# Optimization experiments

Measured on AMD Instinct MI355X. Metric: run time of the kernel, lower is better.

The kernel has to match this reference:

```python
import jax, jax.numpy as jnp
import numpy as np

EMBED_DIM = 2048
N_HEAD = 16
N_KV_HEAD = 4
HEAD_DIM = EMBED_DIM // N_HEAD  # 128
GROUP = N_HEAD // N_KV_HEAD     # 4
SCALE = HEAD_DIM ** -0.5
B, T = 2, 2048


def setup_inputs() -> dict:
    key = jax.random.key(0)
    ks = jax.random.split(key, 5)
    s = 0.02
    # weights stored as [in, out] (y = x @ W); equivalent to torch Linear W.T
    return {
        "x": jax.random.normal(ks[0], (B, T, EMBED_DIM), jnp.float32),
        "Wq": jax.random.normal(ks[1], (EMBED_DIM, EMBED_DIM), jnp.float32) * s,
        "Wk": jax.random.normal(ks[2], (EMBED_DIM, N_KV_HEAD * HEAD_DIM), jnp.float32) * s,
        "Wv": jax.random.normal(ks[3], (EMBED_DIM, N_KV_HEAD * HEAD_DIM), jnp.float32) * s,
        "Wo": jax.random.normal(ks[4], (EMBED_DIM, EMBED_DIM), jnp.float32) * s,
    }


def reference(x, Wq, Wk, Wv, Wo):
    # Prefill path (T>1, no cache): GQA causal attention, eval mode (dropout=0).
    Bq, Tq, C = x.shape
    q = (x @ Wq).reshape(Bq, Tq, N_HEAD, HEAD_DIM).transpose(0, 2, 1, 3)      # (B,Hq,T,D)
    k = (x @ Wk).reshape(Bq, Tq, N_KV_HEAD, HEAD_DIM).transpose(0, 2, 1, 3)  # (B,Hkv,T,D)
    v = (x @ Wv).reshape(Bq, Tq, N_KV_HEAD, HEAD_DIM).transpose(0, 2, 1, 3)
    # expand_kv: each kv head repeated GROUP times consecutively
    k = jnp.repeat(k, GROUP, axis=1)  # (B,Hq,T,D)
    v = jnp.repeat(v, GROUP, axis=1)
    scores = jnp.einsum("bhqd,bhkd->bhqk", q, k) * SCALE
    causal = jnp.tril(jnp.ones((Tq, Tq), dtype=bool))
    scores = jnp.where(causal[None, None], scores, jnp.finfo(scores.dtype).min)
    probs = jax.nn.softmax(scores, axis=-1)
    atten = jnp.einsum("bhqk,bhkd->bhqd", probs, v)
    atten = atten.transpose(0, 2, 1, 3).reshape(Bq, Tq, C)
    out = atten @ Wo
    return out
```

## Files before the change

kernel.cpp:

```cpp
#include <hip/hip_runtime.h>

typedef unsigned short u16;
typedef unsigned int   u32;
typedef __attribute__((ext_vector_type(4))) float  f32x4;
typedef __attribute__((ext_vector_type(8))) __bf16 bf16x8;

#define EMBED 2048
#define NH    16
#define NKV   4
#define HD    128
#define TT    2048
#define BB    2
#define MROWS (BB*TT)
#define QSCALE 0.08838834764831845f

#define QELEMS ((size_t)BB*NH*TT*HD)
#define KELEMS ((size_t)BB*NKV*TT*HD)

static __device__ __forceinline__ u16 f2b(float f){
  union { float f; u32 u; } v; v.f = f;
  u32 u = v.u;
  u32 r = u + 0x7FFFu + ((u >> 16) & 1u);
  return (u16)(r >> 16);
}

__global__ __launch_bounds__(256) void cvt_f32_bf16(const float* __restrict__ in,
                                                    u16* __restrict__ out, int n4){
  int i = blockIdx.x * 256 + threadIdx.x;
  if (i >= n4) return;
  float4 v = ((const float4*)in)[i];
  uint2 o;
  o.x = (u32)f2b(v.x) | ((u32)f2b(v.y) << 16);
  o.y = (u32)f2b(v.z) | ((u32)f2b(v.w) << 16);
  ((uint2*)out)[i] = o;
}

__global__ __launch_bounds__(256) void trans_w2(const float* __restrict__ in0, u16* __restrict__ out0,
                                                const float* __restrict__ in1, u16* __restrict__ out1,
                                                int R, int C){
  const float* in = blockIdx.z ? in1 : in0;
  u16*        out = blockIdx.z ? out1 : out0;
  __shared__ u16 tile[32][33];
  int c0 = blockIdx.x * 32, r0 = blockIdx.y * 32;
  int tx = threadIdx.x & 31, ty = threadIdx.x >> 5;
  #pragma unroll
  for (int j = 0; j < 32; j += 8)
    tile[ty + j][tx] = f2b(in[(size_t)(r0 + ty + j) * C + c0 + tx]);
  __syncthreads();
  #pragma unroll
  for (int j = 0; j < 32; j += 8)
    out[(size_t)(c0 + ty + j) * R + r0 + tx] = tile[tx][ty + j];
}

__global__ __launch_bounds__(256) void trans_v(const u16* __restrict__ in,
                                               u16* __restrict__ out){
  __shared__ u16 tile[32][33];
  int d0 = (blockIdx.x & 3) * 32;
  int t0 = ((blockIdx.x >> 2) & 63) * 32;
  int bh = blockIdx.x >> 8;
  const u16* ip = in  + (size_t)bh * TT * HD;
  u16*       op = out + (size_t)bh * TT * HD;
  int tx = threadIdx.x & 31, ty = threadIdx.x >> 5;
  #pragma unroll
  for (int j = 0; j < 32; j += 8)
    tile[ty + j][tx] = ip[(size_t)(t0 + ty + j) * HD + d0 + tx];
  __syncthreads();
  #pragma unroll
  for (int j = 0; j < 32; j += 8)
    op[(size_t)(d0 + ty + j) * TT + t0 + tx] = tile[tx][ty + j];
}

template<int EPI>
__global__ __launch_bounds__(256)
void gemm_bt(const u16* __restrict__ A, const u16* __restrict__ Bt,
             void* __restrict__ outp, int N, int K){
  __shared__ __align__(16) u16 As[2][128*32];
  __shared__ __align__(16) u16 Bs[2][128*32];
  int tid  = threadIdx.x;
  int lane = tid & 63, w = tid >> 6;
  int nwg = gridDim.x;
  int bid = blockIdx.x;
  bid = (bid & 7) * (nwg >> 3) + (bid >> 3);
  int nbn  = N >> 7;
  int brow = (bid / nbn) * 128;
  int bcol = (bid % nbn) * 128;

  auto stage = [&](int buf, int kt){
    #pragma unroll
    for (int j = 0; j < 2; ++j){
      int boff  = w * 2048 + j * 1024;
      int chunk = (boff >> 4) + lane;
      int row   = chunk >> 2;
      int cko   = chunk & 3;
      const u16* ga = A  + (size_t)(brow + row) * K + kt + cko * 8;
      const u16* gb = Bt + (size_t)(bcol + row) * K + kt + cko * 8;
      __builtin_amdgcn_global_load_lds((__attribute__((address_space(1))) void*)(void*)ga,
          (__attribute__((address_space(3))) void*)(void*)(&As[buf][boff >> 1]), 16, 0, 0);
      __builtin_amdgcn_global_load_lds((__attribute__((address_space(1))) void*)(void*)gb,
          (__attribute__((address_space(3))) void*)(void*)(&Bs[buf][boff >> 1]), 16, 0, 0);
    }
  };

  int lr = lane & 15, lg = lane >> 4, lk = lg * 8;
  int wr = (w >> 1) * 64, wc = (w & 1) * 64;

  f32x4 acc[4][4];
  #pragma unroll
  for (int m = 0; m < 4; ++m)
    #pragma unroll
    for (int n = 0; n < 4; ++n)
      #pragma unroll
      for (int r = 0; r < 4; ++r) acc[m][n][r] = 0.f;

  int NT = K >> 5;
  stage(0, 0);
  asm volatile("s_waitcnt vmcnt(0)" ::: "memory");
  __syncthreads();
  int cur = 0;
  for (int t = 0; t < NT; ++t){
    if (t + 1 < NT) stage(cur ^ 1, (t + 1) * 32);
    const u16* as = As[cur];
    const u16* bs = Bs[cur];
    bf16x8 af[4], bfv[4];
    #pragma unroll
    for (int m = 0; m < 4; ++m) af[m]  = *(const bf16x8*)(as + (wr + m*16 + lr)*32 + lk);
    #pragma unroll
    for (int n = 0; n < 4; ++n) bfv[n] = *(const bf16x8*)(bs + (wc + n*16 + lr)*32 + lk);
    #pragma unroll
    for (int m = 0; m < 4; ++m)
      #pragma unroll
      for (int n = 0; n < 4; ++n)
        acc[m][n] = __builtin_amdgcn_mfma_f32_16x16x32_bf16(af[m], bfv[n], acc[m][n], 0, 0, 0);
    asm volatile("s_waitcnt vmcnt(0)" ::: "memory");
    __syncthreads();
    cur ^= 1;
  }

  if (EPI == 0){
    float* o = (float*)outp;
    #pragma unroll
    for (int m = 0; m < 4; ++m)
      #pragma unroll
      for (int r = 0; r < 4; ++r){
        int rowg = brow + wr + m*16 + lg*4 + r;
        float* orow = o + (size_t)rowg * N + bcol + wc + lr;
        #pragma unroll
        for (int n = 0; n < 4; ++n) orow[n*16] = acc[m][n][r];
      }
  } else {
    u16* qb = (u16*)outp;
    u16* kb = qb + QELEMS;
    u16* vb = kb + KELEMS;
    int hb = bcol >> 7;
    int b  = brow >> 11;
    u16* hp; float s;
    if (hb < 16)      { hp = qb + ((size_t)(b*NH  +  hb     )) * TT * HD; s = QSCALE; }
    else if (hb < 20) { hp = kb + ((size_t)(b*NKV + (hb-16))) * TT * HD; s = 1.0f; }
    else              { hp = vb + ((size_t)(b*NKV + (hb-20))) * TT * HD; s = 1.0f; }
    #pragma unroll
    for (int m = 0; m < 4; ++m)
      #pragma unroll
      for (int r = 0; r < 4; ++r){
        int t = (brow + wr + m*16 + lg*4 + r) & (TT - 1);
        #pragma unroll
        for (int n = 0; n < 4; ++n){
          int d = wc + n*16 + lr;
          hp[(size_t)t * HD + d] = f2b(acc[m][n][r] * s);
        }
      }
  }
}

__global__ __launch_bounds__(256)
void attn_kernel(const u16* __restrict__ qb, const u16* __restrict__ kb,
                 const u16* __restrict__ vtb, u16* __restrict__ ob){
  __shared__ __align__(16) u16 Ks[2][64*128];
  __shared__ __align__(16) u16 Vs[2][128*64];
  __shared__ __align__(16) u16 pl[4][16*88];
  int tid = threadIdx.x, lane = tid & 63, w = tid >> 6;
  int nwg = gridDim.x;
  int bid = blockIdx.x;
  bid = (bid & 7) * (nwg >> 3) + (bid >> 3);
  int pair = bid & 15;
  int h    = (bid >> 4) & 15;
  int b    = bid >> 8;
  int hkv  = h >> 2;
  int lr = lane & 15, lg = lane >> 4, lk = lg * 8;
  int sw = (lr & 7) << 3;

  const u16* qbase = qb  + ((size_t)b * NH  + h  ) * TT * HD;
  const u16* kbase = kb  + ((size_t)b * NKV + hkv) * TT * HD;
  const u16* vbase = vtb + ((size_t)b * NKV + hkv) * HD * TT;

  auto stage = [&](int buf, int kt){
    #pragma unroll
    for (int i = 0; i < 4; ++i){
      int c  = i * 256 + tid;
      int ub = (i * 256 + w * 64) * 8;
      int kr = c >> 4, kc = (c & 15) ^ (kr & 7);
      const u16* gk = kbase + (size_t)(kt * 64 + kr) * HD + kc * 8;
      __builtin_amdgcn_global_load_lds((__attribute__((address_space(1))) void*)(void*)gk,
          (__attribute__((address_space(3))) void*)(void*)(&Ks[buf][ub]), 16, 0, 0);
      int vr = c >> 3, vc = (c & 7) ^ (vr & 7);
      const u16* gv = vbase + (size_t)vr * TT + kt * 64 + vc * 8;
      __builtin_amdgcn_global_load_lds((__attribute__((address_space(1))) void*)(void*)gv,
          (__attribute__((address_space(3))) void*)(void*)(&Vs[buf][ub]), 16, 0, 0);
    }
  };

  __bf16* plw = (__bf16*)pl[w];

  for (int half = 0; half < 2; ++half){
    int qt = half ? (31 - pair) : pair;
    int q0 = qt * 64 + w * 16;

    bf16x8 aq[4];
    #pragma unroll
    for (int s = 0; s < 4; ++s)
      aq[s] = *(const bf16x8*)(qbase + (size_t)(q0 + lr) * HD + s*32 + lk);

    f32x4 o_acc[8];
    #pragma unroll
    for (int dt = 0; dt < 8; ++dt)
      #pragma unroll
      for (int r = 0; r < 4; ++r) o_acc[dt][r] = 0.f;
    float mrow[4], lrow[4];
    #pragma unroll
    for (int r = 0; r < 4; ++r){ mrow[r] = -1e30f; lrow[r] = 0.f; }

    __builtin_amdgcn_s_barrier();
    stage(0, 0);
    int cur = 0;
    for (int kt = 0; kt <= qt; ++kt){
      __builtin_amdgcn_s_barrier();
      if (kt < qt){
        stage(cur ^ 1, kt + 1);
        asm volatile("s_waitcnt vmcnt(8)" ::: "memory");
      } else {
        asm volatile("s_waitcnt vmcnt(0)" ::: "memory");
      }
      __builtin_amdgcn_s_barrier();

      const u16* ks = Ks[cur];
      f32x4 sc[4];
      #pragma unroll
      for (int c = 0; c < 4; ++c)
        #pragma unroll
        for (int r = 0; r < 4; ++r) sc[c][r] = 0.f;
      __builtin_amdgcn_s_setprio(1);
      #pragma unroll
      for (int c = 0; c < 4; ++c){
        const u16* kp = ks + (c*16 + lr) * 128;
        #pragma unroll
        for (int s = 0; s < 4; ++s){
          bf16x8 kf = *(const bf16x8*)(kp + (((s*32) + lk) ^ sw));
          sc[c] = __builtin_amdgcn_mfma_f32_16x16x32_bf16(aq[s], kf, sc[c], 0, 0, 0);
        }
      }
      __builtin_amdgcn_s_setprio(0);
      if (kt == qt){
        #pragma unroll
        for (int c = 0; c < 4; ++c){
          int kvg = kt*64 + c*16 + lr;
          #pragma unroll
          for (int r = 0; r < 4; ++r){
            int qg = q0 + lg*4 + r;
            if (kvg > qg) sc[c][r] = -1e30f;
          }
        }
      }
      float tmv[4];
      #pragma unroll
      for (int r = 0; r < 4; ++r){
        float tm = fmaxf(fmaxf(sc[0][r], sc[1][r]), fmaxf(sc[2][r], sc[3][r]));
        tm = fmaxf(tm, __shfl_xor(tm, 1));
        tm = fmaxf(tm, __shfl_xor(tm, 2));
        tm = fmaxf(tm, __shfl_xor(tm, 4));
        tm = fmaxf(tm, __shfl_xor(tm, 8));
        tmv[r] = tm;
      }
      bool need = (tmv[0] > mrow[0] + 8.f) || (tmv[1] > mrow[1] + 8.f) ||
                  (tmv[2] > mrow[2] + 8.f) || (tmv[3] > mrow[3] + 8.f);
      if (__any(need ? 1 : 0)){
        #pragma unroll
        for (int r = 0; r < 4; ++r){
          float mnew  = fmaxf(mrow[r], tmv[r]);
          float alpha = __expf(mrow[r] - mnew);
          mrow[r] = mnew;
          lrow[r] *= alpha;
          #pragma unroll
          for (int dt = 0; dt < 8; ++dt) o_acc[dt][r] *= alpha;
        }
      }
      #pragma unroll
      for (int r = 0; r < 4; ++r){
        float rs = 0.f;
        #pragma unroll
        for (int c = 0; c < 4; ++c){
          float p = __expf(sc[c][r] - mrow[r]);
          rs += p;
          plw[(lg*4 + r)*88 + c*16 + lr] = (__bf16)p;
        }
        rs += __shfl_xor(rs, 1); rs += __shfl_xor(rs, 2);
        rs += __shfl_xor(rs, 4); rs += __shfl_xor(rs, 8);
        lrow[r] += rs;
      }
      asm volatile("s_waitcnt lgkmcnt(0)" ::: "memory");
      bf16x8 pa[2];
      #pragma unroll
      for (int kk = 0; kk < 2; ++kk)
        pa[kk] = *(const bf16x8*)((const u16*)plw + lr*88 + kk*32 + lk);
      const u16* vs = Vs[cur];
      __builtin_amdgcn_s_setprio(1);
      #pragma unroll
      for (int dt = 0; dt < 8; ++dt){
        const u16* vp = vs + (dt*16 + lr) * 64;
        #pragma unroll
        for (int kk = 0; kk < 2; ++kk){
          bf16x8 vf = *(const bf16x8*)(vp + (((kk*32) + lk) ^ sw));
          o_acc[dt] = __builtin_amdgcn_mfma_f32_16x16x32_bf16(pa[kk], vf, o_acc[dt], 0, 0, 0);
        }
      }
      __builtin_amdgcn_s_setprio(0);
      cur ^= 1;
    }
    #pragma unroll
    for (int r = 0; r < 4; ++r){
      float inv = 1.0f / lrow[r];
      int t = q0 + lg*4 + r;
      size_t base = ((size_t)b * TT + t) * EMBED + h * HD;
      #pragma unroll
      for (int dt = 0; dt < 8; ++dt)
        ob[base + dt*16 + lr] = f2b(o_acc[dt][r] * inv);
    }
  }
}

extern "C" void kernel_launch(void* const* d_in, const int* in_sizes, int n_in,
                              void* d_out, int out_size, void* d_ws, size_t ws_size,
                              hipStream_t stream){
  const float* x  = (const float*)d_in[0];
  const float* Wq = (const float*)d_in[1];
  const float* Wk = (const float*)d_in[2];
  const float* Wv = (const float*)d_in[3];
  const float* Wo = (const float*)d_in[4];

  char* ws = (char*)d_ws;
  size_t off = 0;
  auto alloc = [&](size_t bytes){ void* p = ws + off; off += (bytes + 255) & ~(size_t)255; return p; };
  u16* xb    = (u16*)alloc((size_t)MROWS * EMBED * 2);
  u16* Wqkvt = (u16*)alloc((size_t)3072 * EMBED * 2);
  u16* Wot   = (u16*)alloc((size_t)EMBED * EMBED * 2);
  u16* qkv   = (u16*)alloc((QELEMS + 2*KELEMS) * 2);
  u16* vtb   = (u16*)alloc(KELEMS * 2);
  u16* ob    = (u16*)alloc((size_t)MROWS * EMBED * 2);

  u16* qb = qkv;
  u16* kb = qb + QELEMS;
  u16* vb = kb + KELEMS;

  cvt_f32_bf16<<<(MROWS*EMBED/4 + 255)/256, 256, 0, stream>>>(x, xb, MROWS*EMBED/4);
  trans_w2<<<dim3(EMBED/32, EMBED/32, 2), 256, 0, stream>>>(Wq, Wqkvt, Wo, Wot, EMBED, EMBED);
  trans_w2<<<dim3(512/32,   EMBED/32, 2), 256, 0, stream>>>(Wk, Wqkvt + (size_t)2048*EMBED,
                                                            Wv, Wqkvt + (size_t)2560*EMBED, EMBED, 512);

  gemm_bt<2><<<(MROWS/128)*(3072/128), 256, 0, stream>>>(xb, Wqkvt, qkv, 3072, EMBED);
  trans_v<<<4*64*BB*NKV, 256, 0, stream>>>(vb, vtb);

  attn_kernel<<<BB*NH*16, 256, 0, stream>>>(qb, kb, vtb, ob);

  gemm_bt<0><<<(MROWS/128)*(EMBED/128), 256, 0, stream>>>(ob, Wot, d_out, EMBED, EMBED);
}
```

Baseline: 313.1 us.

## Use 256x256-tile 8-wave GEMM with swizzled LDS and phased prefetch for QKV

The QKV projection moves from the 128x128 tile, 4-wave GEMM to a new 256x256 tile kernel with 512 threads. It uses a two-half K=64 step, XOR-swizzled LDS layout, prefetch split across barriered phases, and s_setprio around the MFMA blocks. The larger tile doubles reuse per LDS load and cuts global traffic, and interleaving the loads with MFMA is meant to hide latency. In exchange it uses more LDS and registers, launches only 192 workgroups, which leaves the 256 CUs under-filled, and adds more barriers. The output GEMM keeps the old kernel, now de-templated.

```diff
diff --git a/kernel.cpp b/kernel.cpp
--- a/kernel.cpp
+++ b/kernel.cpp
@@ -16,6 +16,9 @@
 
 #define QELEMS ((size_t)BB*NH*TT*HD)
 #define KELEMS ((size_t)BB*NKV*TT*HD)
+
+#define AS1(p) (__attribute__((address_space(1))) void*)(void*)(p)
+#define AS3(p) (__attribute__((address_space(3))) void*)(void*)(p)
 
 static __device__ __forceinline__ u16 f2b(float f){
   union { float f; u32 u; } v; v.f = f;
@@ -70,7 +73,6 @@
     op[(size_t)(d0 + ty + j) * TT + t0 + tx] = tile[tx][ty + j];
 }
 
-template<int EPI>
 __global__ __launch_bounds__(256)
 void gemm_bt(const u16* __restrict__ A, const u16* __restrict__ Bt,
              void* __restrict__ outp, int N, int K){
@@ -94,10 +96,8 @@
       int cko   = chunk & 3;
       const u16* ga = A  + (size_t)(brow + row) * K + kt + cko * 8;
       const u16* gb = Bt + (size_t)(bcol + row) * K + kt + cko * 8;
-      __builtin_amdgcn_global_load_lds((__attribute__((address_space(1))) void*)(void*)ga,
-          (__attribute__((address_space(3))) void*)(void*)(&As[buf][boff >> 1]), 16, 0, 0);
-      __builtin_amdgcn_global_load_lds((__attribute__((address_space(1))) void*)(void*)gb,
-          (__attribute__((address_space(3))) void*)(void*)(&Bs[buf][boff >> 1]), 16, 0, 0);
+      __builtin_amdgcn_global_load_lds(AS1(ga), AS3(&As[buf][boff >> 1]), 16, 0, 0);
+      __builtin_amdgcn_global_load_lds(AS1(gb), AS3(&Bs[buf][boff >> 1]), 16, 0, 0);
     }
   };
 
@@ -136,39 +136,152 @@
     cur ^= 1;
   }
 
-  if (EPI == 0){
-    float* o = (float*)outp;
+  float* o = (float*)outp;
+  #pragma unroll
+  for (int m = 0; m < 4; ++m)
+    #pragma unroll
+    for (int r = 0; r < 4; ++r){
+      int rowg = brow + wr + m*16 + lg*4 + r;
+      float* orow = o + (size_t)rowg * N + bcol + wc + lr;
+      #pragma unroll
+      for (int n = 0; n < 4; ++n) orow[n*16] = acc[m][n][r];
+    }
+}
+
+__global__ __launch_bounds__(512, 2)
+void gemm256_qkv(const u16* __restrict__ A, const u16* __restrict__ Bt,
+                 u16* __restrict__ qkv, int N, int K){
+  __shared__ __align__(16) u16 As[2][2][256*32];
+  __shared__ __align__(16) u16 Bs[2][2][256*32];
+  int tid = threadIdx.x, lane = tid & 63, w = tid >> 6;
+  int nwg = gridDim.x, bid = blockIdx.x;
+  bid = (bid & 7) * (nwg >> 3) + (bid >> 3);
+  int nbn  = N >> 8;
+  int brow = (bid / nbn) * 256;
+  int bcol = (bid % nbn) * 256;
+  int wm = w >> 2, wn = w & 3;
+  int lr = lane & 15, lg = lane >> 4;
+  int swz = (lg ^ ((lr >> 1) & 3)) << 3;
+
+  auto stage = [&](const u16* __restrict__ src, u16* dst, int rowbase, int kt, int kk){
+    #pragma unroll
+    for (int j = 0; j < 2; ++j){
+      int c = j * 512 + tid;
+      int row = c >> 2, cc = c & 3;
+      const u16* g = src + (size_t)(rowbase + row) * K + kt * 64 + kk * 32
+                         + ((cc ^ ((row >> 1) & 3)) * 8);
+      __builtin_amdgcn_global_load_lds(AS1(g), AS3(dst + (j * 512 + w * 64) * 8), 16, 0, 0);
+    }
+  };
+
+  f32x4 acc[8][4];
+  #pragma unroll
+  for (int m = 0; m < 8; ++m)
+    #pragma unroll
+    for (int n = 0; n < 4; ++n)
+      #pragma unroll
+      for (int r = 0; r < 4; ++r) acc[m][n][r] = 0.f;
+
+  int NT = K >> 6;
+  int arow = wm * 128 + lr;
+  int brw  = wn * 64 + lr;
+
+  stage(A,  As[0][0], brow, 0, 0);
+  stage(Bt, Bs[0][0], bcol, 0, 0);
+  stage(A,  As[0][1], brow, 0, 1);
+  stage(Bt, Bs[0][1], bcol, 0, 1);
+  asm volatile("s_waitcnt vmcnt(4)" ::: "memory");
+  __builtin_amdgcn_s_barrier();
+  asm volatile("" ::: "memory");
+
+  for (int t = 0; t < NT; ++t){
+    int buf = t & 1, nb = buf ^ 1;
+    bool pre = (t + 1 < NT);
+    const u16* a0 = As[buf][0]; const u16* b0 = Bs[buf][0];
+    const u16* a1 = As[buf][1]; const u16* b1 = Bs[buf][1];
+    bf16x8 bfr[4], af[4];
+
+    #pragma unroll
+    for (int n = 0; n < 4; ++n) bfr[n] = *(const bf16x8*)(b0 + (brw + n*16)*32 + swz);
+    #pragma unroll
+    for (int m = 0; m < 4; ++m) af[m]  = *(const bf16x8*)(a0 + (arow + m*16)*32 + swz);
+    if (pre) stage(A, As[nb][0], brow, t + 1, 0);
+    __builtin_amdgcn_s_barrier(); asm volatile("" ::: "memory");
+    __builtin_amdgcn_s_setprio(1);
     #pragma unroll
     for (int m = 0; m < 4; ++m)
       #pragma unroll
-      for (int r = 0; r < 4; ++r){
-        int rowg = brow + wr + m*16 + lg*4 + r;
-        float* orow = o + (size_t)rowg * N + bcol + wc + lr;
-        #pragma unroll
-        for (int n = 0; n < 4; ++n) orow[n*16] = acc[m][n][r];
-      }
-  } else {
-    u16* qb = (u16*)outp;
-    u16* kb = qb + QELEMS;
-    u16* vb = kb + KELEMS;
-    int hb = bcol >> 7;
-    int b  = brow >> 11;
-    u16* hp; float s;
-    if (hb < 16)      { hp = qb + ((size_t)(b*NH  +  hb     )) * TT * HD; s = QSCALE; }
-    else if (hb < 20) { hp = kb + ((size_t)(b*NKV + (hb-16))) * TT * HD; s = 1.0f; }
-    else              { hp = vb + ((size_t)(b*NKV + (hb-20))) * TT * HD; s = 1.0f; }
+      for (int n = 0; n < 4; ++n)
+        acc[m][n] = __builtin_amdgcn_mfma_f32_16x16x32_bf16(af[m], bfr[n], acc[m][n], 0, 0, 0);
+    __builtin_amdgcn_s_setprio(0);
+    __builtin_amdgcn_s_barrier(); asm volatile("" ::: "memory");
+
+    #pragma unroll
+    for (int m = 0; m < 4; ++m) af[m] = *(const bf16x8*)(a0 + (arow + (m+4)*16)*32 + swz);
+    if (pre) stage(Bt, Bs[nb][0], bcol, t + 1, 0);
+    __builtin_amdgcn_s_barrier(); asm volatile("" ::: "memory");
+    __builtin_amdgcn_s_setprio(1);
     #pragma unroll
     for (int m = 0; m < 4; ++m)
       #pragma unroll
-      for (int r = 0; r < 4; ++r){
-        int t = (brow + wr + m*16 + lg*4 + r) & (TT - 1);
-        #pragma unroll
-        for (int n = 0; n < 4; ++n){
-          int d = wc + n*16 + lr;
-          hp[(size_t)t * HD + d] = f2b(acc[m][n][r] * s);
-        }
-      }
+      for (int n = 0; n < 4; ++n)
+        acc[m+4][n] = __builtin_amdgcn_mfma_f32_16x16x32_bf16(af[m], bfr[n], acc[m+4][n], 0, 0, 0);
+    __builtin_amdgcn_s_setprio(0);
+    if (pre) asm volatile("s_waitcnt vmcnt(4)" ::: "memory");
+    else     asm volatile("s_waitcnt vmcnt(0)" ::: "memory");
+    __builtin_amdgcn_s_barrier(); asm volatile("" ::: "memory");
+
+    #pragma unroll
+    for (int n = 0; n < 4; ++n) bfr[n] = *(const bf16x8*)(b1 + (brw + n*16)*32 + swz);
+    #pragma unroll
+    for (int m = 0; m < 4; ++m) af[m]  = *(const bf16x8*)(a1 + (arow + m*16)*32 + swz);
+    if (pre) stage(A, As[nb][1], brow, t + 1, 1);
+    __builtin_amdgcn_s_barrier(); asm volatile("" ::: "memory");
+    __builtin_amdgcn_s_setprio(1);
+    #pragma unroll
+    for (int m = 0; m < 4; ++m)
+      #pragma unroll
+      for (int n = 0; n < 4; ++n)
+        acc[m][n] = __builtin_amdgcn_mfma_f32_16x16x32_bf16(af[m], bfr[n], acc[m][n], 0, 0, 0);
+    __builtin_amdgcn_s_setprio(0);
+    __builtin_amdgcn_s_barrier(); asm volatile("" ::: "memory");
+
+    #pragma unroll
+    for (int m = 0; m < 4; ++m) af[m] = *(const bf16x8*)(a1 + (arow + (m+4)*16)*32 + swz);
+    if (pre) stage(Bt, Bs[nb][1], bcol, t + 1, 1);
+    __builtin_amdgcn_s_barrier(); asm volatile("" ::: "memory");
+    __builtin_amdgcn_s_setprio(1);
+    #pragma unroll
+    for (int m = 0; m < 4; ++m)
+      #pragma unroll
+      for (int n = 0; n < 4; ++n)
+        acc[m+4][n] = __builtin_amdgcn_mfma_f32_16x16x32_bf16(af[m], bfr[n], acc[m+4][n], 0, 0, 0);
+    __builtin_amdgcn_s_setprio(0);
+    if (pre) asm volatile("s_waitcnt vmcnt(4)" ::: "memory");
+    __builtin_amdgcn_s_barrier(); asm volatile("" ::: "memory");
   }
+
+  u16* qb = qkv;
+  u16* kb = qb + QELEMS;
+  u16* vb = kb + KELEMS;
+  int colbase = bcol + wn * 64;
+  int hb = colbase >> 7;
+  int dbase = colbase & 127;
+  int b = brow >> 11;
+  u16* hp; float s;
+  if (hb < 16)      { hp = qb + ((size_t)(b*NH  +  hb     )) * TT * HD; s = QSCALE; }
+  else if (hb < 20) { hp = kb + ((size_t)(b*NKV + (hb-16))) * TT * HD; s = 1.0f; }
+  else              { hp = vb + ((size_t)(b*NKV + (hb-20))) * TT * HD; s = 1.0f; }
+  #pragma unroll
+  for (int m = 0; m < 8; ++m)
+    #pragma unroll
+    for (int r = 0; r < 4; ++r){
+      int trow = (brow + wm*128 + m*16 + lg*4 + r) & (TT - 1);
+      u16* orow = hp + (size_t)trow * HD + dbase + lr;
+      #pragma unroll
+      for (int n = 0; n < 4; ++n)
+        orow[n*16] = f2b(acc[m][n][r] * s);
+    }
 }
 
 __global__ __launch_bounds__(256)
@@ -199,12 +312,10 @@
       int ub = (i * 256 + w * 64) * 8;
       int kr = c >> 4, kc = (c & 15) ^ (kr & 7);
       const u16* gk = kbase + (size_t)(kt * 64 + kr) * HD + kc * 8;
-      __builtin_amdgcn_global_load_lds((__attribute__((address_space(1))) void*)(void*)gk,
-          (__attribute__((address_space(3))) void*)(void*)(&Ks[buf][ub]), 16, 0, 0);
+      __builtin_amdgcn_global_load_lds(AS1(gk), AS3(&Ks[buf][ub]), 16, 0, 0);
       int vr = c >> 3, vc = (c & 7) ^ (vr & 7);
       const u16* gv = vbase + (size_t)vr * TT + kt * 64 + vc * 8;
-      __builtin_amdgcn_global_load_lds((__attribute__((address_space(1))) void*)(void*)gv,
-          (__attribute__((address_space(3))) void*)(void*)(&Vs[buf][ub]), 16, 0, 0);
+      __builtin_amdgcn_global_load_lds(AS1(gv), AS3(&Vs[buf][ub]), 16, 0, 0);
     }
   };
 
@@ -364,10 +475,10 @@
   trans_w2<<<dim3(512/32,   EMBED/32, 2), 256, 0, stream>>>(Wk, Wqkvt + (size_t)2048*EMBED,
                                                             Wv, Wqkvt + (size_t)2560*EMBED, EMBED, 512);
 
-  gemm_bt<2><<<(MROWS/128)*(3072/128), 256, 0, stream>>>(xb, Wqkvt, qkv, 3072, EMBED);
+  gemm256_qkv<<<(MROWS/256)*(3072/256), 512, 0, stream>>>(xb, Wqkvt, qkv, 3072, EMBED);
   trans_v<<<4*64*BB*NKV, 256, 0, stream>>>(vb, vtb);
 
   attn_kernel<<<BB*NH*16, 256, 0, stream>>>(qb, kb, vtb, ob);
 
-  gemm_bt<0><<<(MROWS/128)*(EMBED/128), 256, 0, stream>>>(ob, Wot, d_out, EMBED, EMBED);
-}
+  gemm_bt<<<(MROWS/128)*(EMBED/128), 256, 0, stream>>>(ob, Wot, d_out, EMBED, EMBED);
+}
```

New measurement: 322.7 us. +3.1%, slower.

## Single-buffer attention LDS and launch one workgroup per query tile

Applied to the files above, without the earlier changes.

The attention kernel drops the double-buffered K/V shared-memory tiles in favour of a single buffer, roughly halving its LDS footprint so more workgroups can be resident per CU. It also stops pairing causal query tiles per workgroup and launches one workgroup per 64-row query tile, doubling the grid. The cost is that K/V loads for the next tile no longer overlap compute: each iteration stages, waits for all loads and barriers. Causal load imbalance across workgroups is now left to the hardware scheduler rather than the paired-tile scheme.

```diff
diff --git a/kernel.cpp b/kernel.cpp
--- a/kernel.cpp
+++ b/kernel.cpp
@@ -16,6 +16,10 @@
 
 #define QELEMS ((size_t)BB*NH*TT*HD)
 #define KELEMS ((size_t)BB*NKV*TT*HD)
+
+#define AS1(p) (__attribute__((address_space(1))) void*)(void*)(p)
+#define AS3(p) (__attribute__((address_space(3))) void*)(void*)(p)
+
 
 static __device__ __forceinline__ u16 f2b(float f){
   union { float f; u32 u; } v; v.f = f;
@@ -94,10 +98,8 @@
       int cko   = chunk & 3;
       const u16* ga = A  + (size_t)(brow + row) * K + kt + cko * 8;
       const u16* gb = Bt + (size_t)(bcol + row) * K + kt + cko * 8;
-      __builtin_amdgcn_global_load_lds((__attribute__((address_space(1))) void*)(void*)ga,
-          (__attribute__((address_space(3))) void*)(void*)(&As[buf][boff >> 1]), 16, 0, 0);
-      __builtin_amdgcn_global_load_lds((__attribute__((address_space(1))) void*)(void*)gb,
-          (__attribute__((address_space(3))) void*)(void*)(&Bs[buf][boff >> 1]), 16, 0, 0);
+      __builtin_amdgcn_global_load_lds(AS1(ga), AS3(&As[buf][boff >> 1]), 16, 0, 0);
+      __builtin_amdgcn_global_load_lds(AS1(gb), AS3(&Bs[buf][boff >> 1]), 16, 0, 0);
     }
   };
 
@@ -174,17 +176,17 @@
 __global__ __launch_bounds__(256)
 void attn_kernel(const u16* __restrict__ qb, const u16* __restrict__ kb,
                  const u16* __restrict__ vtb, u16* __restrict__ ob){
-  __shared__ __align__(16) u16 Ks[2][64*128];
-  __shared__ __align__(16) u16 Vs[2][128*64];
+  __shared__ __align__(16) u16 Ks[64*128];
+  __shared__ __align__(16) u16 Vs[128*64];
   __shared__ __align__(16) u16 pl[4][16*88];
   int tid = threadIdx.x, lane = tid & 63, w = tid >> 6;
   int nwg = gridDim.x;
   int bid = blockIdx.x;
   bid = (bid & 7) * (nwg >> 3) + (bid >> 3);
-  int pair = bid & 15;
-  int h    = (bid >> 4) & 15;
-  int b    = bid >> 8;
-  int hkv  = h >> 2;
+  int qt = bid & 31;
+  int h  = (bid >> 5) & 15;
+  int b  = bid >> 9;
+  int hkv = h >> 2;
   int lr = lane & 15, lg = lane >> 4, lk = lg * 8;
   int sw = (lr & 7) << 3;
 
@@ -192,147 +194,136 @@
   const u16* kbase = kb  + ((size_t)b * NKV + hkv) * TT * HD;
   const u16* vbase = vtb + ((size_t)b * NKV + hkv) * HD * TT;
 
-  auto stage = [&](int buf, int kt){
+  auto stage = [&](int kt){
     #pragma unroll
     for (int i = 0; i < 4; ++i){
       int c  = i * 256 + tid;
       int ub = (i * 256 + w * 64) * 8;
       int kr = c >> 4, kc = (c & 15) ^ (kr & 7);
       const u16* gk = kbase + (size_t)(kt * 64 + kr) * HD + kc * 8;
-      __builtin_amdgcn_global_load_lds((__attribute__((address_space(1))) void*)(void*)gk,
-          (__attribute__((address_space(3))) void*)(void*)(&Ks[buf][ub]), 16, 0, 0);
+      __builtin_amdgcn_global_load_lds(AS1(gk), AS3(&Ks[ub]), 16, 0, 0);
       int vr = c >> 3, vc = (c & 7) ^ (vr & 7);
       const u16* gv = vbase + (size_t)vr * TT + kt * 64 + vc * 8;
-      __builtin_amdgcn_global_load_lds((__attribute__((address_space(1))) void*)(void*)gv,
-          (__attribute__((address_space(3))) void*)(void*)(&Vs[buf][ub]), 16, 0, 0);
+      __builtin_amdgcn_global_load_lds(AS1(gv), AS3(&Vs[ub]), 16, 0, 0);
     }
   };
 
   __bf16* plw = (__bf16*)pl[w];
-
-  for (int half = 0; half < 2; ++half){
-    int qt = half ? (31 - pair) : pair;
-    int q0 = qt * 64 + w * 16;
-
-    bf16x8 aq[4];
-    #pragma unroll
-    for (int s = 0; s < 4; ++s)
-      aq[s] = *(const bf16x8*)(qbase + (size_t)(q0 + lr) * HD + s*32 + lk);
-
-    f32x4 o_acc[8];
-    #pragma unroll
-    for (int dt = 0; dt < 8; ++dt)
-      #pragma unroll
-      for (int r = 0; r < 4; ++r) o_acc[dt][r] = 0.f;
-    float mrow[4], lrow[4];
-    #pragma unroll
-    for (int r = 0; r < 4; ++r){ mrow[r] = -1e30f; lrow[r] = 0.f; }
-
-    __builtin_amdgcn_s_barrier();
-    stage(0, 0);
-    int cur = 0;
-    for (int kt = 0; kt <= qt; ++kt){
-      __builtin_amdgcn_s_barrier();
-      if (kt < qt){
-        stage(cur ^ 1, kt + 1);
-        asm volatile("s_waitcnt vmcnt(8)" ::: "memory");
-      } else {
-        asm volatile("s_waitcnt vmcnt(0)" ::: "memory");
-      }
-      __builtin_amdgcn_s_barrier();
-
-      const u16* ks = Ks[cur];
-      f32x4 sc[4];
-      #pragma unroll
-      for (int c = 0; c < 4; ++c)
-        #pragma unroll
-        for (int r = 0; r < 4; ++r) sc[c][r] = 0.f;
-      __builtin_amdgcn_s_setprio(1);
+  int q0 = qt * 64 + w * 16;
+
+  bf16x8 aq[4];
+  #pragma unroll
+  for (int s = 0; s < 4; ++s)
+    aq[s] = *(const bf16x8*)(qbase + (size_t)(q0 + lr) * HD + s*32 + lk);
+
+  f32x4 o_acc[8];
+  #pragma unroll
+  for (int dt = 0; dt < 8; ++dt)
+    #pragma unroll
+    for (int r = 0; r < 4; ++r) o_acc[dt][r] = 0.f;
+  float mrow[4], lrow[4];
+  #pragma unroll
+  for (int r = 0; r < 4; ++r){ mrow[r] = -1e30f; lrow[r] = 0.f; }
+
+  stage(0);
+  asm volatile("s_waitcnt vmcnt(0)" ::: "memory");
+  __builtin_amdgcn_s_barrier();
+
+  for (int kt = 0; kt <= qt; ++kt){
+    f32x4 sc[4];
+    #pragma unroll
+    for (int c = 0; c < 4; ++c)
+      #pragma unroll
+      for (int r = 0; r < 4; ++r) sc[c][r] = 0.f;
+    __builtin_amdgcn_s_setprio(1);
+    #pragma unroll
+    for (int c = 0; c < 4; ++c){
+      const u16* kp = Ks + (c*16 + lr) * 128;
+      #pragma unroll
+      for (int s = 0; s < 4; ++s){
+        bf16x8 kf = *(const bf16x8*)(kp + (((s*32) + lk) ^ sw));
+        sc[c] = __builtin_amdgcn_mfma_f32_16x16x32_bf16(aq[s], kf, sc[c], 0, 0, 0);
+      }
+    }
+    __builtin_amdgcn_s_setprio(0);
+    if (kt == qt){
       #pragma unroll
       for (int c = 0; c < 4; ++c){
-        const u16* kp = ks + (c*16 + lr) * 128;
-        #pragma unroll
-        for (int s = 0; s < 4; ++s){
-          bf16x8 kf = *(const bf16x8*)(kp + (((s*32) + lk) ^ sw));
-          sc[c] = __builtin_amdgcn_mfma_f32_16x16x32_bf16(aq[s], kf, sc[c], 0, 0, 0);
-        }
-      }
-      __builtin_amdgcn_s_setprio(0);
-      if (kt == qt){
-        #pragma unroll
-        for (int c = 0; c < 4; ++c){
-          int kvg = kt*64 + c*16 + lr;
-          #pragma unroll
-          for (int r = 0; r < 4; ++r){
-            int qg = q0 + lg*4 + r;
-            if (kvg > qg) sc[c][r] = -1e30f;
-          }
-        }
-      }
-      float tmv[4];
-      #pragma unroll
-      for (int r = 0; r < 4; ++r){
-        float tm = fmaxf(fmaxf(sc[0][r], sc[1][r]), fmaxf(sc[2][r], sc[3][r]));
-        tm = fmaxf(tm, __shfl_xor(tm, 1));
-        tm = fmaxf(tm, __shfl_xor(tm, 2));
-        tm = fmaxf(tm, __shfl_xor(tm, 4));
-        tm = fmaxf(tm, __shfl_xor(tm, 8));
-        tmv[r] = tm;
-      }
-      bool need = (tmv[0] > mrow[0] + 8.f) || (tmv[1] > mrow[1] + 8.f) ||
-                  (tmv[2] > mrow[2] + 8.f) || (tmv[3] > mrow[3] + 8.f);
-      if (__any(need ? 1 : 0)){
+        int kvg = kt*64 + c*16 + lr;
         #pragma unroll
         for (int r = 0; r < 4; ++r){
-          float mnew  = fmaxf(mrow[r], tmv[r]);
-          float alpha = __expf(mrow[r] - mnew);
-          mrow[r] = mnew;
-          lrow[r] *= alpha;
-          #pragma unroll
-          for (int dt = 0; dt < 8; ++dt) o_acc[dt][r] *= alpha;
+          int qg = q0 + lg*4 + r;
+          if (kvg > qg) sc[c][r] = -1e30f;
         }
       }
+    }
+    float tmv[4];
+    #pragma unroll
+    for (int r = 0; r < 4; ++r){
+      float tm = fmaxf(fmaxf(sc[0][r], sc[1][r]), fmaxf(sc[2][r], sc[3][r]));
+      tm = fmaxf(tm, __shfl_xor(tm, 1));
+      tm = fmaxf(tm, __shfl_xor(tm, 2));
+      tm = fmaxf(tm, __shfl_xor(tm, 4));
+      tm = fmaxf(tm, __shfl_xor(tm, 8));
+      tmv[r] = tm;
+    }
+    bool need = (tmv[0] > mrow[0] + 8.f) || (tmv[1] > mrow[1] + 8.f) ||
+                (tmv[2] > mrow[2] + 8.f) || (tmv[3] > mrow[3] + 8.f);
+    if (__any(need ? 1 : 0)){
       #pragma unroll
       for (int r = 0; r < 4; ++r){
-        float rs = 0.f;
+        float mnew  = fmaxf(mrow[r], tmv[r]);
+        float alpha = __expf(mrow[r] - mnew);
+        mrow[r] = mnew;
+        lrow[r] *= alpha;
         #pragma unroll
-        for (int c = 0; c < 4; ++c){
-          float p = __expf(sc[c][r] - mrow[r]);
-          rs += p;
-          plw[(lg*4 + r)*88 + c*16 + lr] = (__bf16)p;
-        }
-        rs += __shfl_xor(rs, 1); rs += __shfl_xor(rs, 2);
-        rs += __shfl_xor(rs, 4); rs += __shfl_xor(rs, 8);
-        lrow[r] += rs;
-      }
-      asm volatile("s_waitcnt lgkmcnt(0)" ::: "memory");
-      bf16x8 pa[2];
-      #pragma unroll
-      for (int kk = 0; kk < 2; ++kk)
-        pa[kk] = *(const bf16x8*)((const u16*)plw + lr*88 + kk*32 + lk);
-      const u16* vs = Vs[cur];
-      __builtin_amdgcn_s_setprio(1);
-      #pragma unroll
-      for (int dt = 0; dt < 8; ++dt){
-        const u16* vp = vs + (dt*16 + lr) * 64;
-        #pragma unroll
-        for (int kk = 0; kk < 2; ++kk){
-          bf16x8 vf = *(const bf16x8*)(vp + (((kk*32) + lk) ^ sw));
-          o_acc[dt] = __builtin_amdgcn_mfma_f32_16x16x32_bf16(pa[kk], vf, o_acc[dt], 0, 0, 0);
-        }
-      }
-      __builtin_amdgcn_s_setprio(0);
-      cur ^= 1;
+        for (int dt = 0; dt < 8; ++dt) o_acc[dt][r] *= alpha;
+      }
     }
     #pragma unroll
     for (int r = 0; r < 4; ++r){
-      float inv = 1.0f / lrow[r];
-      int t = q0 + lg*4 + r;
-      size_t base = ((size_t)b * TT + t) * EMBED + h * HD;
-      #pragma unroll
-      for (int dt = 0; dt < 8; ++dt)
-        ob[base + dt*16 + lr] = f2b(o_acc[dt][r] * inv);
-    }
+      float rs = 0.f;
+      #pragma unroll
+      for (int c = 0; c < 4; ++c){
+        float p = __expf(sc[c][r] - mrow[r]);
+        rs += p;
+        plw[(lg*4 + r)*88 + c*16 + lr] = (__bf16)p;
+      }
+      rs += __shfl_xor(rs, 1); rs += __shfl_xor(rs, 2);
+      rs += __shfl_xor(rs, 4); rs += __shfl_xor(rs, 8);
+      lrow[r] += rs;
+    }
+    asm volatile("s_waitcnt lgkmcnt(0)" ::: "memory");
+    bf16x8 pa[2];
+    #pragma unroll
+    for (int kk = 0; kk < 2; ++kk)
+      pa[kk] = *(const bf16x8*)((const u16*)plw + lr*88 + kk*32 + lk);
+    __builtin_amdgcn_s_setprio(1);
+    #pragma unroll
+    for (int dt = 0; dt < 8; ++dt){
+      const u16* vp = Vs + (dt*16 + lr) * 64;
+      #pragma unroll
+      for (int kk = 0; kk < 2; ++kk){
+        bf16x8 vf = *(const bf16x8*)(vp + (((kk*32) + lk) ^ sw));
+        o_acc[dt] = __builtin_amdgcn_mfma_f32_16x16x32_bf16(pa[kk], vf, o_acc[dt], 0, 0, 0);
+      }
+    }
+    __builtin_amdgcn_s_setprio(0);
+    if (kt < qt){
+      __builtin_amdgcn_s_barrier();
+      stage(kt + 1);
+      asm volatile("s_waitcnt vmcnt(0)" ::: "memory");
+      __builtin_amdgcn_s_barrier();
+    }
+  }
+  #pragma unroll
+  for (int r = 0; r < 4; ++r){
+    float inv = 1.0f / lrow[r];
+    int t = q0 + lg*4 + r;
+    size_t base = ((size_t)b * TT + t) * EMBED + h * HD;
+    #pragma unroll
+    for (int dt = 0; dt < 8; ++dt)
+      ob[base + dt*16 + lr] = f2b(o_acc[dt][r] * inv);
   }
 }
 
@@ -367,7 +358,7 @@
   gemm_bt<2><<<(MROWS/128)*(3072/128), 256, 0, stream>>>(xb, Wqkvt, qkv, 3072, EMBED);
   trans_v<<<4*64*BB*NKV, 256, 0, stream>>>(vb, vtb);
 
-  attn_kernel<<<BB*NH*16, 256, 0, stream>>>(qb, kb, vtb, ob);
+  attn_kernel<<<BB*NH*32, 256, 0, stream>>>(qb, kb, vtb, ob);
 
   gemm_bt<0><<<(MROWS/128)*(EMBED/128), 256, 0, stream>>>(ob, Wot, d_out, EMBED, EMBED);
 }
```

After: 341.2 us. 9.0% more time.

## Compute transposed QK^T scores and pass P to PV MFMA via register shuffles

Applied to the files above, without the earlier changes.

Swaps the MFMA operand order so each lane holds scores for a single query row across 16 keys, making the row max/sum reductions cheaper (two cross-group shuffles instead of four-step xor trees per row). The LDS round-trip for the probability tile is replaced by packed bf16 conversion and cross-lane shuffles that assemble the PV A-operand directly in registers. This removes the per-wave LDS buffer and the lgkmcnt wait, at the cost of extra shuffles and selects, and per-row alpha and l values that now have to be broadcast back to the accumulator layout.

```diff
diff --git a/kernel.cpp b/kernel.cpp
--- a/kernel.cpp
+++ b/kernel.cpp
@@ -16,6 +16,10 @@
 
 #define QELEMS ((size_t)BB*NH*TT*HD)
 #define KELEMS ((size_t)BB*NKV*TT*HD)
+
+#define AS1(p) (__attribute__((address_space(1))) void*)(void*)(p)
+#define AS3(p) (__attribute__((address_space(3))) void*)(void*)(p)
+
 
 static __device__ __forceinline__ u16 f2b(float f){
   union { float f; u32 u; } v; v.f = f;
@@ -94,10 +98,8 @@
       int cko   = chunk & 3;
       const u16* ga = A  + (size_t)(brow + row) * K + kt + cko * 8;
       const u16* gb = Bt + (size_t)(bcol + row) * K + kt + cko * 8;
-      __builtin_amdgcn_global_load_lds((__attribute__((address_space(1))) void*)(void*)ga,
-          (__attribute__((address_space(3))) void*)(void*)(&As[buf][boff >> 1]), 16, 0, 0);
-      __builtin_amdgcn_global_load_lds((__attribute__((address_space(1))) void*)(void*)gb,
-          (__attribute__((address_space(3))) void*)(void*)(&Bs[buf][boff >> 1]), 16, 0, 0);
+      __builtin_amdgcn_global_load_lds(AS1(ga), AS3(&As[buf][boff >> 1]), 16, 0, 0);
+      __builtin_amdgcn_global_load_lds(AS1(gb), AS3(&Bs[buf][boff >> 1]), 16, 0, 0);
     }
   };
 
@@ -176,7 +178,6 @@
                  const u16* __restrict__ vtb, u16* __restrict__ ob){
   __shared__ __align__(16) u16 Ks[2][64*128];
   __shared__ __align__(16) u16 Vs[2][128*64];
-  __shared__ __align__(16) u16 pl[4][16*88];
   int tid = threadIdx.x, lane = tid & 63, w = tid >> 6;
   int nwg = gridDim.x;
   int bid = blockIdx.x;
@@ -185,8 +186,9 @@
   int h    = (bid >> 4) & 15;
   int b    = bid >> 8;
   int hkv  = h >> 2;
-  int lr = lane & 15, lg = lane >> 4, lk = lg * 8;
-  int sw = (lr & 7) << 3;
+  int j  = lane & 15, g = lane >> 4, lk = g * 8;
+  int gh = g >> 1;
+  int sw = (j & 7) << 3;
 
   const u16* qbase = qb  + ((size_t)b * NH  + h  ) * TT * HD;
   const u16* kbase = kb  + ((size_t)b * NKV + hkv) * TT * HD;
@@ -199,16 +201,12 @@
       int ub = (i * 256 + w * 64) * 8;
       int kr = c >> 4, kc = (c & 15) ^ (kr & 7);
       const u16* gk = kbase + (size_t)(kt * 64 + kr) * HD + kc * 8;
-      __builtin_amdgcn_global_load_lds((__attribute__((address_space(1))) void*)(void*)gk,
-          (__attribute__((address_space(3))) void*)(void*)(&Ks[buf][ub]), 16, 0, 0);
+      __builtin_amdgcn_global_load_lds(AS1(gk), AS3(&Ks[buf][ub]), 16, 0, 0);
       int vr = c >> 3, vc = (c & 7) ^ (vr & 7);
       const u16* gv = vbase + (size_t)vr * TT + kt * 64 + vc * 8;
-      __builtin_amdgcn_global_load_lds((__attribute__((address_space(1))) void*)(void*)gv,
-          (__attribute__((address_space(3))) void*)(void*)(&Vs[buf][ub]), 16, 0, 0);
+      __builtin_amdgcn_global_load_lds(AS1(gv), AS3(&Vs[buf][ub]), 16, 0, 0);
     }
   };
-
-  __bf16* plw = (__bf16*)pl[w];
 
   for (int half = 0; half < 2; ++half){
     int qt = half ? (31 - pair) : pair;
@@ -217,16 +215,14 @@
     bf16x8 aq[4];
     #pragma unroll
     for (int s = 0; s < 4; ++s)
-      aq[s] = *(const bf16x8*)(qbase + (size_t)(q0 + lr) * HD + s*32 + lk);
+      aq[s] = *(const bf16x8*)(qbase + (size_t)(q0 + j) * HD + s*32 + lk);
 
     f32x4 o_acc[8];
     #pragma unroll
     for (int dt = 0; dt < 8; ++dt)
       #pragma unroll
       for (int r = 0; r < 4; ++r) o_acc[dt][r] = 0.f;
-    float mrow[4], lrow[4];
-    #pragma unroll
-    for (int r = 0; r < 4; ++r){ mrow[r] = -1e30f; lrow[r] = 0.f; }
+    float mrow = -1e30f, lrow = 0.f;
 
     __builtin_amdgcn_s_barrier();
     stage(0, 0);
@@ -250,71 +246,78 @@
       __builtin_amdgcn_s_setprio(1);
       #pragma unroll
       for (int c = 0; c < 4; ++c){
-        const u16* kp = ks + (c*16 + lr) * 128;
+        const u16* kp = ks + (c*16 + j) * 128;
         #pragma unroll
         for (int s = 0; s < 4; ++s){
           bf16x8 kf = *(const bf16x8*)(kp + (((s*32) + lk) ^ sw));
-          sc[c] = __builtin_amdgcn_mfma_f32_16x16x32_bf16(aq[s], kf, sc[c], 0, 0, 0);
+          sc[c] = __builtin_amdgcn_mfma_f32_16x16x32_bf16(kf, aq[s], sc[c], 0, 0, 0);
         }
       }
       __builtin_amdgcn_s_setprio(0);
       if (kt == qt){
-        #pragma unroll
-        for (int c = 0; c < 4; ++c){
-          int kvg = kt*64 + c*16 + lr;
+        int qg = q0 + j;
+        #pragma unroll
+        for (int c = 0; c < 4; ++c)
           #pragma unroll
-          for (int r = 0; r < 4; ++r){
-            int qg = q0 + lg*4 + r;
-            if (kvg > qg) sc[c][r] = -1e30f;
-          }
-        }
-      }
-      float tmv[4];
-      #pragma unroll
-      for (int r = 0; r < 4; ++r){
-        float tm = fmaxf(fmaxf(sc[0][r], sc[1][r]), fmaxf(sc[2][r], sc[3][r]));
-        tm = fmaxf(tm, __shfl_xor(tm, 1));
-        tm = fmaxf(tm, __shfl_xor(tm, 2));
-        tm = fmaxf(tm, __shfl_xor(tm, 4));
-        tm = fmaxf(tm, __shfl_xor(tm, 8));
-        tmv[r] = tm;
-      }
-      bool need = (tmv[0] > mrow[0] + 8.f) || (tmv[1] > mrow[1] + 8.f) ||
-                  (tmv[2] > mrow[2] + 8.f) || (tmv[3] > mrow[3] + 8.f);
-      if (__any(need ? 1 : 0)){
+          for (int r = 0; r < 4; ++r)
+            if (kt*64 + c*16 + g*4 + r > qg) sc[c][r] = -1e30f;
+      }
+      float tm = fmaxf(fmaxf(fmaxf(sc[0][0], sc[0][1]), fmaxf(sc[0][2], sc[0][3])),
+                       fmaxf(fmaxf(sc[1][0], sc[1][1]), fmaxf(sc[1][2], sc[1][3])));
+      tm = fmaxf(tm, fmaxf(fmaxf(fmaxf(sc[2][0], sc[2][1]), fmaxf(sc[2][2], sc[2][3])),
+                           fmaxf(fmaxf(sc[3][0], sc[3][1]), fmaxf(sc[3][2], sc[3][3]))));
+      tm = fmaxf(tm, __shfl_xor(tm, 16));
+      tm = fmaxf(tm, __shfl_xor(tm, 32));
+      if (__any((tm > mrow + 8.f) ? 1 : 0)){
+        float mnew  = fmaxf(mrow, tm);
+        float alpha = __expf(mrow - mnew);
+        mrow = mnew;
+        lrow *= alpha;
         #pragma unroll
         for (int r = 0; r < 4; ++r){
-          float mnew  = fmaxf(mrow[r], tmv[r]);
-          float alpha = __expf(mrow[r] - mnew);
-          mrow[r] = mnew;
-          lrow[r] *= alpha;
+          float ar = __shfl(alpha, (lane & 48) | (g*4 + r));
           #pragma unroll
-          for (int dt = 0; dt < 8; ++dt) o_acc[dt][r] *= alpha;
-        }
-      }
-      #pragma unroll
-      for (int r = 0; r < 4; ++r){
-        float rs = 0.f;
-        #pragma unroll
-        for (int c = 0; c < 4; ++c){
-          float p = __expf(sc[c][r] - mrow[r]);
+          for (int dt = 0; dt < 8; ++dt) o_acc[dt][r] *= ar;
+        }
+      }
+      float rs = 0.f;
+      #pragma unroll
+      for (int c = 0; c < 4; ++c)
+        #pragma unroll
+        for (int r = 0; r < 4; ++r){
+          float p = __expf(sc[c][r] - mrow);
+          sc[c][r] = p;
           rs += p;
-          plw[(lg*4 + r)*88 + c*16 + lr] = (__bf16)p;
-        }
-        rs += __shfl_xor(rs, 1); rs += __shfl_xor(rs, 2);
-        rs += __shfl_xor(rs, 4); rs += __shfl_xor(rs, 8);
-        lrow[r] += rs;
-      }
-      asm volatile("s_waitcnt lgkmcnt(0)" ::: "memory");
+        }
+      rs += __shfl_xor(rs, 16);
+      rs += __shfl_xor(rs, 32);
+      lrow += rs;
+      u32 pk[4][2];
+      #pragma unroll
+      for (int c = 0; c < 4; ++c){
+        asm("v_cvt_pk_bf16_f32 %0, %1, %2" : "=v"(pk[c][0]) : "v"(sc[c][0]), "v"(sc[c][1]));
+        asm("v_cvt_pk_bf16_f32 %0, %1, %2" : "=v"(pk[c][1]) : "v"(sc[c][2]), "v"(sc[c][3]));
+      }
       bf16x8 pa[2];
       #pragma unroll
-      for (int kk = 0; kk < 2; ++kk)
-        pa[kk] = *(const bf16x8*)((const u16*)plw + lr*88 + kk*32 + lk);
+      for (int kk = 0; kk < 2; ++kk){
+        u32 a0 = pk[2*kk + gh][0],       a1 = pk[2*kk + gh][1];
+        u32 b0 = pk[2*kk + (gh ^ 1)][0], b1 = pk[2*kk + (gh ^ 1)][1];
+        u32 v16_0 = (u32)__shfl_xor((int)a0, 16), v16_1 = (u32)__shfl_xor((int)a1, 16);
+        u32 v32_0 = (u32)__shfl_xor((int)b0, 32), v32_1 = (u32)__shfl_xor((int)b1, 32);
+        u32 v48_0 = (u32)__shfl_xor((int)b0, 48), v48_1 = (u32)__shfl_xor((int)b1, 48);
+        union { u32 uw[4]; bf16x8 v; } u;
+        u.uw[0] = (g==0) ? pk[2*kk][0]   : (g==1) ? v48_0 : (g==2) ? v32_0 : v16_0;
+        u.uw[1] = (g==0) ? pk[2*kk][1]   : (g==1) ? v48_1 : (g==2) ? v32_1 : v16_1;
+        u.uw[2] = (g==0) ? v16_0 : (g==1) ? v32_0 : (g==2) ? v48_0 : pk[2*kk+1][0];
+        u.uw[3] = (g==0) ? v16_1 : (g==1) ? v32_1 : (g==2) ? v48_1 : pk[2*kk+1][1];
+        pa[kk] = u.v;
+      }
       const u16* vs = Vs[cur];
       __builtin_amdgcn_s_setprio(1);
       #pragma unroll
       for (int dt = 0; dt < 8; ++dt){
-        const u16* vp = vs + (dt*16 + lr) * 64;
+        const u16* vp = vs + (dt*16 + j) * 64;
         #pragma unroll
         for (int kk = 0; kk < 2; ++kk){
           bf16x8 vf = *(const bf16x8*)(vp + (((kk*32) + lk) ^ sw));
@@ -326,12 +329,13 @@
     }
     #pragma unroll
     for (int r = 0; r < 4; ++r){
-      float inv = 1.0f / lrow[r];
-      int t = q0 + lg*4 + r;
+      float ls  = __shfl(lrow, (lane & 48) | (g*4 + r));
+      float inv = 1.0f / ls;
+      int t = q0 + g*4 + r;
       size_t base = ((size_t)b * TT + t) * EMBED + h * HD;
       #pragma unroll
       for (int dt = 0; dt < 8; ++dt)
-        ob[base + dt*16 + lr] = f2b(o_acc[dt][r] * inv);
+        ob[base + dt*16 + j] = f2b(o_acc[dt][r] * inv);
     }
   }
 }
```

Result: no change. 313.3 us (+0.1%).
